# Kernel optimization log

Measured on AMD Instinct MI355X. Metric: run time of the kernel, lower is better.

## Reference

```python
import jax, jax.numpy as jnp
import numpy as np

DIM = 1024
HEADS = 16
HEAD_DIM = DIM // HEADS
RANK = 16
ALPHA = 8.0
SCALING = ALPHA / RANK  # 0.5
SCALE = HEAD_DIM ** (-0.5)
B_, L_ = 2, 2048


def _proj_params(key, std=0.02):
    kW, kb, kA, kB = jax.random.split(key, 4)
    W = jax.random.normal(kW, (DIM, DIM), jnp.float32) * std   # [out, in]
    b = jax.random.normal(kb, (DIM,), jnp.float32) * std
    A = jax.random.normal(kA, (DIM, RANK), jnp.float32) * std  # [out, r]
    Bm = jax.random.normal(kB, (RANK, DIM), jnp.float32) * std # [r, in]
    return W, b, A, Bm


def setup_inputs() -> dict:
    key = jax.random.key(0)
    ks = jax.random.split(key, 6)
    x = jax.random.normal(ks[0], (B_, L_, DIM), jnp.float32)
    attn_bias = jax.random.normal(ks[1], (1, HEADS, L_, L_), jnp.float32) * 0.1
    inp = {"x": x, "attn_bias": attn_bias}
    for name, k in zip("qkvo", ks[2:6]):
        W, b, A, Bm = _proj_params(k)
        inp[f"W{name}"] = W
        inp[f"b{name}"] = b
        inp[f"A{name}"] = A
        inp[f"B{name}"] = Bm
    return inp


def _lora_linear(x, W, b, A, Bm):
    # y = x W^T + b + scaling * ((x @ A) @ B)   (matches torch LoRALinear)
    return x @ W.T + b + SCALING * ((x @ A) @ Bm)


def _split(x):
    B, L, D = x.shape
    return jnp.swapaxes(x.reshape(B, L, HEADS, HEAD_DIM), 1, 2)  # [B,H,L,hd]


def reference(x, attn_bias, Wq, bq, Aq, Bq, Wk, bk, Ak, Bk, Wv, bv, Av, Bv, Wo, bo, Ao, Bo):
    B, L, D = x.shape
    q = _split(_lora_linear(x, Wq, bq, Aq, Bq))
    k = _split(_lora_linear(x, Wk, bk, Ak, Bk))
    v = _split(_lora_linear(x, Wv, bv, Av, Bv))
    scores = jnp.einsum('bhld,bhmd->bhlm', q, k) * SCALE + attn_bias
    attn = jax.nn.softmax(scores, axis=-1)  # dropout p=0 -> identity
    out = jnp.einsum('bhlm,bhmd->bhld', attn, v)
    out = jnp.swapaxes(out, 1, 2).reshape(B, L, D)  # merge heads
    return _lora_linear(out, Wo, bo, Ao, Bo)
```

## Files before the change

kernel.cpp:

```cpp
#include <hip/hip_runtime.h>
#include <cstdint>

typedef __bf16 bf16;
typedef __bf16 bf16x8 __attribute__((ext_vector_type(8)));
typedef __bf16 bf16x4 __attribute__((ext_vector_type(4)));
typedef float  f32x4  __attribute__((ext_vector_type(4)));
typedef float  f32x16 __attribute__((ext_vector_type(16)));
typedef int    i32x4  __attribute__((ext_vector_type(4)));

#define DIM   1024
#define LSEQ  2048
#define NH    16
#define HD    64
#define NTOK  4096

#define AS1C(p) ((const __attribute__((address_space(1))) void*)(unsigned long long)(uintptr_t)(p))
#define AS3P(p) ((__attribute__((address_space(3))) void*)(unsigned int)(uintptr_t)(p))
#define SB0 __builtin_amdgcn_sched_barrier(0)
#define CPOL_NT 2

__device__ __forceinline__ f32x4 mfma16(bf16x8 a, bf16x8 b, f32x4 c) {
  return __builtin_amdgcn_mfma_f32_16x16x32_bf16(a, b, c, 0, 0, 0);
}
__device__ __forceinline__ f32x16 mfma32(bf16x8 a, bf16x8 b, f32x16 c) {
  return __builtin_amdgcn_mfma_f32_32x32x16_bf16(a, b, c, 0, 0, 0);
}
__device__ __forceinline__ int pk2(float a, float b) {
  unsigned short ua = __builtin_bit_cast(unsigned short, (bf16)a);
  unsigned short ub = __builtin_bit_cast(unsigned short, (bf16)b);
  return (int)ua | ((int)ub << 16);
}

__global__ __launch_bounds__(256) void k_cvt(const float* __restrict__ x,
                                             bf16* __restrict__ xb) {
  const int i = (blockIdx.x * 256 + threadIdx.x) * 4;
  const f32x4 v = *(const f32x4*)(x + i);
  bf16x4 o;
  o[0] = (bf16)v[0]; o[1] = (bf16)v[1]; o[2] = (bf16)v[2]; o[3] = (bf16)v[3];
  *(bf16x4*)(xb + i) = o;
}

struct WeffArgs {
  const float* W[4]; const float* A[4]; const float* B[4]; bf16* out[4];
};

__global__ __launch_bounds__(256) void k_weff(WeffArgs args) {
  const int o = blockIdx.x;
  const int z = blockIdx.y;
  const float* __restrict__ W  = args.W[z];
  const float* __restrict__ A  = args.A[z];
  const float* __restrict__ Bm = args.B[z];
  bf16* __restrict__ out = args.out[z];
  float Bo[16];
#pragma unroll
  for (int r = 0; r < 16; ++r) Bo[r] = Bm[r * DIM + o];
#pragma unroll
  for (int j = 0; j < 4; ++j) {
    const int d = j * 256 + (int)threadIdx.x;
    const float* Ar = A + (size_t)d * 16;
    float acc = 0.f;
#pragma unroll
    for (int r = 0; r < 16; ++r) acc += Ar[r] * Bo[r];
    out[(size_t)o * DIM + d] = (bf16)(W[(size_t)o * DIM + d] + 0.5f * acc);
  }
}

template <int NF, bool F32OUT>
__device__ __forceinline__ void gemm_body64(const bf16* __restrict__ X,
                                            const bf16* __restrict__ W,
                                            const float* __restrict__ bias,
                                            void* __restrict__ out,
                                            float scale, int m0, int n0, int ncol0) {
  constexpr int BN = NF * 32;
  constexpr int BJ = BN / 32;
  __shared__ __align__(16) bf16 As[128 * 64];
  __shared__ __align__(16) bf16 Bs[BN * 64];
  const int tid  = threadIdx.x;
  const int lane = tid & 63, w = tid >> 6;
  const int l15 = lane & 15, l4 = lane >> 4;
  const int wr = w >> 1, wc = w & 1;
  const int lr = lane >> 3;
  const int scol = ((lane & 7) ^ lr) * 8;

  f32x4 acc[4][NF] = {};
  const bf16* ag = X + (size_t)m0 * DIM;
  const bf16* bg = W + (size_t)n0 * DIM;

  for (int kt = 0; kt < DIM / 64; ++kt) {
    const int k0 = kt * 64;
#pragma unroll
    for (int j = 0; j < 4; ++j) {
      const int rb = w * 4 + j;
      __builtin_amdgcn_global_load_lds(
          AS1C(ag + (size_t)(rb * 8 + lr) * DIM + k0 + scol),
          AS3P(As + rb * 512), 16, 0, 0);
    }
#pragma unroll
    for (int j = 0; j < BJ; ++j) {
      const int rb = w * BJ + j;
      __builtin_amdgcn_global_load_lds(
          AS1C(bg + (size_t)(rb * 8 + lr) * DIM + k0 + scol),
          AS3P(Bs + rb * 512), 16, 0, 0);
    }
    __syncthreads();
    bf16x8 af[2][4], bfr[2][NF];
#pragma unroll
    for (int ks = 0; ks < 2; ++ks) {
#pragma unroll
      for (int m = 0; m < 4; ++m) {
        const int r = wr * 64 + m * 16 + l15;
        af[ks][m] = *(const bf16x8*)(As + r * 64 + ((ks * 4 + l4) ^ (r & 7)) * 8);
      }
#pragma unroll
      for (int n = 0; n < NF; ++n) {
        const int r = wc * (NF * 16) + n * 16 + l15;
        bfr[ks][n] = *(const bf16x8*)(Bs + r * 64 + ((ks * 4 + l4) ^ (r & 7)) * 8);
      }
    }
#pragma unroll
    for (int m = 0; m < 4; ++m)
#pragma unroll
      for (int n = 0; n < NF; ++n) {
        acc[m][n] = mfma16(af[0][m], bfr[0][n], acc[m][n]);
        acc[m][n] = mfma16(af[1][m], bfr[1][n], acc[m][n]);
      }
    __syncthreads();
  }

#pragma unroll
  for (int m = 0; m < 4; ++m) {
    const int r0 = m0 + wr * 64 + m * 16 + l4 * 4;
#pragma unroll
    for (int n = 0; n < NF; ++n) {
      const int c = ncol0 + wc * (NF * 16) + n * 16 + l15;
      const float bc = bias[c];
#pragma unroll
      for (int t = 0; t < 4; ++t) {
        const float y = (acc[m][n][t] + bc) * scale;
        if constexpr (F32OUT)
          ((float*)out)[(size_t)(r0 + t) * DIM + c] = y;
        else
          ((bf16*)out)[(size_t)(r0 + t) * DIM + c] = (bf16)y;
      }
    }
  }
}

__global__ __launch_bounds__(256) void k_gemm_qkv(
    const bf16* __restrict__ xb, const bf16* __restrict__ weff,
    const float* __restrict__ bq, const float* __restrict__ bk,
    const float* __restrict__ bv,
    bf16* __restrict__ q, bf16* __restrict__ k, bf16* __restrict__ v) {
  const int n0 = blockIdx.y * 128;
  const int z = n0 >> 10;
  const float* bias = (z == 0) ? bq : (z == 1) ? bk : bv;
  bf16* out = (z == 0) ? q : (z == 1) ? k : v;
  const float scale = (z == 0) ? 0.125f : 1.0f;
  gemm_body64<4, false>(xb, weff, bias, out, scale, blockIdx.x * 128, n0, n0 & 1023);
}

__global__ __launch_bounds__(256) void k_gemm_o(
    const bf16* __restrict__ ctx, const bf16* __restrict__ weffo,
    const float* __restrict__ bo, float* __restrict__ out) {
  const int n0 = blockIdx.y * 64;
  gemm_body64<2, true>(ctx, weffo, bo, out, 1.0f, blockIdx.x * 128, n0, n0);
}

__global__ __launch_bounds__(256) void k_vfrag(const bf16* __restrict__ v,
                                               const bf16* __restrict__ k,
                                               bf16* __restrict__ vf,
                                               bf16* __restrict__ kf) {
  const int lt = blockIdx.x, bh = blockIdx.y;
  const int b = bh >> 4, h = bh & 15;
  __shared__ __align__(16) bf16 tile[64][72];
  const int tid = threadIdx.x;
  const int r = tid >> 2, c0 = (tid & 3) * 16;
  const bf16* src = v + (size_t)(b * LSEQ + lt * 64) * DIM + h * HD;
  *(bf16x8*)(&tile[r][c0])     = *(const bf16x8*)(src + (size_t)r * DIM + c0);
  *(bf16x8*)(&tile[r][c0 + 8]) = *(const bf16x8*)(src + (size_t)r * DIM + c0 + 8);
  __syncthreads();
  const int w = tid >> 6, lane = tid & 63, l31 = lane & 31, hi = lane >> 5;
  {
    const int tt = w >> 1, n = w & 1;
    const int t = lt * 2 + tt;
#pragma unroll
    for (int c = 0; c < 2; ++c) {
      bf16 tmp[8];
#pragma unroll
      for (int j = 0; j < 8; ++j)
        tmp[j] = tile[tt * 32 + c * 16 + hi * 8 + j][n * 32 + l31];
      *(bf16x8*)(vf + ((((size_t)bh * 64 + t) * 4 + n * 2 + c) * 64 + lane) * 8) =
          *(bf16x8*)tmp;
    }
  }
  {
    const int t = lt * 2 + (w & 1);
    const bf16* krow = k + (size_t)(b * LSEQ + t * 32 + l31) * DIM + h * HD + hi * 8;
#pragma unroll
    for (int cc = 0; cc < 2; ++cc) {
      const int c = (w >> 1) + cc * 2;
      *(bf16x8*)(kf + ((((size_t)bh * 64 + t) * 4 + c) * 64 + lane) * 8) =
          *(const bf16x8*)(krow + c * 16);
    }
  }
}

__global__ __launch_bounds__(512, 4) void k_attn(
    const bf16* __restrict__ q, const bf16* __restrict__ kf,
    const bf16* __restrict__ vf, const float* __restrict__ bias,
    bf16* __restrict__ ctx) {
  const int tid = threadIdx.x, w = tid >> 6, lane = tid & 63;
  const int l31 = lane & 31, hi = lane >> 5;
  const int bb = w >> 2, qs = w & 3;
  const int h = blockIdx.x & 15;
  const int q0 = (blockIdx.x >> 4) * 128;

  __shared__ __align__(16) bf16  kls[2][2][2048];
  __shared__ __align__(16) bf16  vls[2][2][2048];
  __shared__ __align__(16) float bls[3][4096];

  const bf16* qrow = q + (size_t)(bb * LSEQ + q0 + qs * 32 + l31) * DIM + h * HD;
  bf16x8 Qf[4];
#pragma unroll
  for (int c = 0; c < 4; ++c) Qf[c] = *(const bf16x8*)(qrow + c * 16 + hi * 8);

  const int kvA = 2 * w, kvB = 2 * w + 1;
  const int kbA = kvA >> 3, vvA = (kvA >> 2) & 1, cA = kvA & 3;
  const int kbB = kvB >> 3, vvB = (kvB >> 2) & 1, cB = kvB & 3;
  const bf16* srcA = (vvA ? vf : kf) + (size_t)(kbA * NH + h) * 64 * 2048 + cA * 512 + lane * 8;
  const bf16* srcB = (vvB ? vf : kf) + (size_t)(kbB * NH + h) * 64 * 2048 + cB * 512 + lane * 8;
  bf16* dstA = (vvA ? &vls[kbA][0][0] : &kls[kbA][0][0]) + cA * 512 + lane * 8;
  bf16* dstB = (vvB ? &vls[kbB][0][0] : &kls[kbB][0][0]) + cB * 512 + lane * 8;
  const int lr = lane >> 3, lc = lane & 7;
  const float* bsA = bias + ((size_t)h * LSEQ + q0 + 16 * w + lr) * LSEQ + 4 * (lc ^ lr);
  const float* bsB = bsA + (size_t)8 * LSEQ;
  float* bdA = &bls[0][0] + (2 * w) * 256 + lane * 4;
  float* bdB = bdA + 256;

  f32x16 acc0 = {}, acc1 = {};
  float mrun = -3e38f, lrun = 0.f;

#define STAGEKV(t_, s_)                                                        \
  {                                                                            \
    __builtin_amdgcn_global_load_lds(AS1C(srcA + (size_t)(t_) * 2048),         \
                                     AS3P(dstA + (s_) * 2048), 16, 0, 0);      \
    __builtin_amdgcn_global_load_lds(AS1C(srcB + (size_t)(t_) * 2048),         \
                                     AS3P(dstB + (s_) * 2048), 16, 0, 0);      \
  }
#define STAGEB(t_, s_)                                                         \
  {                                                                            \
    __builtin_amdgcn_global_load_lds(AS1C(bsA + (size_t)(t_) * 32),            \
                                     AS3P(bdA + (s_) * 4096), 16, 0, CPOL_NT); \
    __builtin_amdgcn_global_load_lds(AS1C(bsB + (size_t)(t_) * 32),            \
                                     AS3P(bdB + (s_) * 4096), 16, 0, CPOL_NT); \
  }

  STAGEKV(0, 0); SB0;
  STAGEB(0, 0); SB0;
  STAGEB(1, 1); SB0;

  const int rr = qs * 32 + l31;
  const int sw = (l31 & 7) << 2;
  for (int t = 0; t < 64; ++t) {
    const int slKV = t & 1;
    const int slB = t % 3;
    { const int tn = (t + 1 > 63) ? 63 : t + 1; STAGEKV(tn, (t + 1) & 1); } SB0;
    { const int tn = (t + 2 > 63) ? 63 : t + 2; STAGEB(tn, (t + 2) % 3); } SB0;
    asm volatile("s_waitcnt vmcnt(6)" ::: "memory");
    __builtin_amdgcn_s_barrier();

    bf16x8 Kf[4], Vf[2][2];
    f32x4 br[4];
#pragma unroll
    for (int c = 0; c < 4; ++c)
      Kf[c] = *(const bf16x8*)(&kls[bb][slKV][c * 512 + lane * 8]);
#pragma unroll
    for (int u = 0; u < 4; ++u)
      Vf[u >> 1][u & 1] = *(const bf16x8*)(&vls[bb][slKV][u * 512 + lane * 8]);
#pragma unroll
    for (int g = 0; g < 4; ++g)
      br[g] = *(const f32x4*)(
          &bls[slB][rr * 32 + (((g << 3) | (hi << 2)) ^ sw)]);
    asm volatile("s_waitcnt lgkmcnt(0)" ::: "memory");
    SB0;
    __builtin_amdgcn_s_barrier();

    f32x16 s = {};
#pragma unroll
    for (int c = 0; c < 4; ++c) s = mfma32(Kf[c], Qf[c], s);
    float p[16];
#pragma unroll
    for (int r = 0; r < 16; ++r) p[r] = s[r] + br[r >> 2][r & 3];
    float m8[8];
#pragma unroll
    for (int i = 0; i < 8; ++i) m8[i] = fmaxf(p[i], p[i + 8]);
    float tm = fmaxf(fmaxf(fmaxf(m8[0], m8[4]), fmaxf(m8[1], m8[5])),
                     fmaxf(fmaxf(m8[2], m8[6]), fmaxf(m8[3], m8[7])));
    tm = fmaxf(tm, __shfl_xor(tm, 32));
    if (!__all(tm <= mrun + 8.0f)) {
      const float mn = fmaxf(mrun, tm);
      const float scl = __expf(mrun - mn);
      mrun = mn;
      lrun *= scl;
#pragma unroll
      for (int r = 0; r < 16; ++r) { acc0[r] *= scl; acc1[r] *= scl; }
    }
#pragma unroll
    for (int r = 0; r < 16; ++r) p[r] = __expf(p[r] - mrun);
    float s8[8];
#pragma unroll
    for (int i = 0; i < 8; ++i) s8[i] = p[i] + p[i + 8];
    float rs = ((s8[0] + s8[1]) + (s8[2] + s8[3])) + ((s8[4] + s8[5]) + (s8[6] + s8[7]));
    rs += __shfl_xor(rs, 32);
    lrun += rs;
#pragma unroll
    for (int c = 0; c < 2; ++c) {
      const int c8 = c * 8;
      const int A0 = pk2(p[c8 + 0], p[c8 + 1]);
      const int A1 = pk2(p[c8 + 2], p[c8 + 3]);
      const int B0 = pk2(p[c8 + 4], p[c8 + 5]);
      const int B1 = pk2(p[c8 + 6], p[c8 + 7]);
      const int pA0 = __shfl_xor(A0, 32), pA1 = __shfl_xor(A1, 32);
      const int pB0 = __shfl_xor(B0, 32), pB1 = __shfl_xor(B1, 32);
      i32x4 fi;
      fi[0] = hi ? pB0 : A0;
      fi[1] = hi ? pB1 : A1;
      fi[2] = hi ? B0 : pA0;
      fi[3] = hi ? B1 : pA1;
      const bf16x8 pf = __builtin_bit_cast(bf16x8, fi);
      acc0 = mfma32(Vf[0][c], pf, acc0);
      acc1 = mfma32(Vf[1][c], pf, acc1);
    }
  }
#undef STAGEKV
#undef STAGEB

  const float inv = 1.0f / lrun;
  bf16* cp = ctx + (size_t)(bb * LSEQ + q0 + qs * 32 + l31) * DIM + h * HD;
#pragma unroll
  for (int r = 0; r < 16; ++r) {
    const int dr = (r & 3) + 8 * (r >> 2) + 4 * hi;
    cp[dr]      = (bf16)(acc0[r] * inv);
    cp[32 + dr] = (bf16)(acc1[r] * inv);
  }
}

extern "C" void kernel_launch(void* const* d_in, const int* in_sizes, int n_in,
                              void* d_out, int out_size, void* d_ws, size_t ws_size,
                              hipStream_t stream) {
  const float* x  = (const float*)d_in[0];
  const float* ab = (const float*)d_in[1];
  const float* Wq = (const float*)d_in[2];  const float* bq = (const float*)d_in[3];
  const float* Aq = (const float*)d_in[4];  const float* Bq = (const float*)d_in[5];
  const float* Wk = (const float*)d_in[6];  const float* bk = (const float*)d_in[7];
  const float* Ak = (const float*)d_in[8];  const float* Bk = (const float*)d_in[9];
  const float* Wv = (const float*)d_in[10]; const float* bv = (const float*)d_in[11];
  const float* Av = (const float*)d_in[12]; const float* Bv = (const float*)d_in[13];
  const float* Wo = (const float*)d_in[14]; const float* bo = (const float*)d_in[15];
  const float* Ao = (const float*)d_in[16]; const float* Bo = (const float*)d_in[17];

  uint8_t* ws = (uint8_t*)d_ws;
  const size_t SZ = (size_t)NTOK * DIM * sizeof(bf16);
  bf16* xb   = (bf16*)(ws + 0 * SZ);
  bf16* weff = (bf16*)(ws + 1 * SZ);
  bf16* qb   = (bf16*)(ws + 2 * SZ);
  bf16* kb   = (bf16*)(ws + 3 * SZ);
  bf16* vb   = (bf16*)(ws + 4 * SZ);
  bf16* kfb  = (bf16*)(ws + 5 * SZ);
  bf16* vfb  = (bf16*)(ws + 6 * SZ);
  bf16* ctx  = (bf16*)(ws + 7 * SZ);

  k_cvt<<<dim3(NTOK * DIM / 1024), 256, 0, stream>>>(x, xb);

  WeffArgs wa;
  wa.W[0] = Wq; wa.A[0] = Aq; wa.B[0] = Bq; wa.out[0] = weff;
  wa.W[1] = Wk; wa.A[1] = Ak; wa.B[1] = Bk; wa.out[1] = weff + (size_t)DIM * DIM;
  wa.W[2] = Wv; wa.A[2] = Av; wa.B[2] = Bv; wa.out[2] = weff + 2 * (size_t)DIM * DIM;
  wa.W[3] = Wo; wa.A[3] = Ao; wa.B[3] = Bo; wa.out[3] = weff + 3 * (size_t)DIM * DIM;
  k_weff<<<dim3(DIM, 4), 256, 0, stream>>>(wa);

  k_gemm_qkv<<<dim3(32, 24), 256, 0, stream>>>(xb, weff, bq, bk, bv, qb, kb, vb);
  k_vfrag<<<dim3(32, 32), 256, 0, stream>>>(vb, kb, vfb, kfb);
  k_attn<<<dim3(256), 512, 0, stream>>>(qb, kfb, vfb, ab, ctx);
  k_gemm_o<<<dim3(32, 16), 256, 0, stream>>>(ctx, weff + 3 * (size_t)DIM * DIM, bo,
                                             (float*)d_out);
}
```

Baseline: 190.0 us.

## Process two query groups per wave in attention to reuse K/V tiles

Each attention block now covers 256 query rows, with every wave computing two 32-row query groups against the same staged K/V fragments. The grid drops to 128 blocks, the bias staging buffer doubles, and the load wait count is raised to match. The aim is to halve K/V global-to-LDS traffic and barrier overhead per query. In exchange it uses more registers and LDS, lowers occupancy (launch bounds set to 1), and launches fewer blocks than there are CUs.

```diff
diff --git a/kernel.cpp b/kernel.cpp
--- a/kernel.cpp
+++ b/kernel.cpp
@@ -205,7 +205,7 @@
   }
 }
 
-__global__ __launch_bounds__(512, 4) void k_attn(
+__global__ __launch_bounds__(512, 1) void k_attn(
     const bf16* __restrict__ q, const bf16* __restrict__ kf,
     const bf16* __restrict__ vf, const float* __restrict__ bias,
     bf16* __restrict__ ctx) {
@@ -213,16 +213,20 @@
   const int l31 = lane & 31, hi = lane >> 5;
   const int bb = w >> 2, qs = w & 3;
   const int h = blockIdx.x & 15;
-  const int q0 = (blockIdx.x >> 4) * 128;
+  const int q0 = (blockIdx.x >> 4) * 256;
 
   __shared__ __align__(16) bf16  kls[2][2][2048];
   __shared__ __align__(16) bf16  vls[2][2][2048];
-  __shared__ __align__(16) float bls[3][4096];
-
-  const bf16* qrow = q + (size_t)(bb * LSEQ + q0 + qs * 32 + l31) * DIM + h * HD;
-  bf16x8 Qf[4];
-#pragma unroll
-  for (int c = 0; c < 4; ++c) Qf[c] = *(const bf16x8*)(qrow + c * 16 + hi * 8);
+  __shared__ __align__(16) float bls[3][8192];
+
+  bf16x8 Qf[2][4];
+#pragma unroll
+  for (int g = 0; g < 2; ++g) {
+    const bf16* qrow =
+        q + (size_t)(bb * LSEQ + q0 + qs * 64 + g * 32 + l31) * DIM + h * HD;
+#pragma unroll
+    for (int c = 0; c < 4; ++c) Qf[g][c] = *(const bf16x8*)(qrow + c * 16 + hi * 8);
+  }
 
   const int kvA = 2 * w, kvB = 2 * w + 1;
   const int kbA = kvA >> 3, vvA = (kvA >> 2) & 1, cA = kvA & 3;
@@ -231,14 +235,19 @@
   const bf16* srcB = (vvB ? vf : kf) + (size_t)(kbB * NH + h) * 64 * 2048 + cB * 512 + lane * 8;
   bf16* dstA = (vvA ? &vls[kbA][0][0] : &kls[kbA][0][0]) + cA * 512 + lane * 8;
   bf16* dstB = (vvB ? &vls[kbB][0][0] : &kls[kbB][0][0]) + cB * 512 + lane * 8;
+
   const int lr = lane >> 3, lc = lane & 7;
-  const float* bsA = bias + ((size_t)h * LSEQ + q0 + 16 * w + lr) * LSEQ + 4 * (lc ^ lr);
-  const float* bsB = bsA + (size_t)8 * LSEQ;
-  float* bdA = &bls[0][0] + (2 * w) * 256 + lane * 4;
-  float* bdB = bdA + 256;
-
-  f32x16 acc0 = {}, acc1 = {};
-  float mrun = -3e38f, lrun = 0.f;
+  const float* bs0 = bias + ((size_t)h * LSEQ + q0 + 32 * w + lr) * LSEQ + 4 * (lc ^ lr);
+  const float* bs1 = bs0 + (size_t)8 * LSEQ;
+  const float* bs2 = bs0 + (size_t)16 * LSEQ;
+  const float* bs3 = bs0 + (size_t)24 * LSEQ;
+  float* bd0 = &bls[0][0] + (4 * w) * 256 + lane * 4;
+  float* bd1 = bd0 + 256;
+  float* bd2 = bd0 + 512;
+  float* bd3 = bd0 + 768;
+
+  f32x16 acc0[2] = {}, acc1[2] = {};
+  float mrun[2] = {-3e38f, -3e38f}, lrun[2] = {0.f, 0.f};
 
 #define STAGEKV(t_, s_)                                                        \
   {                                                                            \
@@ -249,28 +258,31 @@
   }
 #define STAGEB(t_, s_)                                                         \
   {                                                                            \
-    __builtin_amdgcn_global_load_lds(AS1C(bsA + (size_t)(t_) * 32),            \
-                                     AS3P(bdA + (s_) * 4096), 16, 0, CPOL_NT); \
-    __builtin_amdgcn_global_load_lds(AS1C(bsB + (size_t)(t_) * 32),            \
-                                     AS3P(bdB + (s_) * 4096), 16, 0, CPOL_NT); \
+    __builtin_amdgcn_global_load_lds(AS1C(bs0 + (size_t)(t_) * 32),            \
+                                     AS3P(bd0 + (s_) * 8192), 16, 0, CPOL_NT); \
+    __builtin_amdgcn_global_load_lds(AS1C(bs1 + (size_t)(t_) * 32),            \
+                                     AS3P(bd1 + (s_) * 8192), 16, 0, CPOL_NT); \
+    __builtin_amdgcn_global_load_lds(AS1C(bs2 + (size_t)(t_) * 32),            \
+                                     AS3P(bd2 + (s_) * 8192), 16, 0, CPOL_NT); \
+    __builtin_amdgcn_global_load_lds(AS1C(bs3 + (size_t)(t_) * 32),            \
+                                     AS3P(bd3 + (s_) * 8192), 16, 0, CPOL_NT); \
   }
 
   STAGEKV(0, 0); SB0;
   STAGEB(0, 0); SB0;
   STAGEB(1, 1); SB0;
 
-  const int rr = qs * 32 + l31;
   const int sw = (l31 & 7) << 2;
   for (int t = 0; t < 64; ++t) {
     const int slKV = t & 1;
     const int slB = t % 3;
     { const int tn = (t + 1 > 63) ? 63 : t + 1; STAGEKV(tn, (t + 1) & 1); } SB0;
     { const int tn = (t + 2 > 63) ? 63 : t + 2; STAGEB(tn, (t + 2) % 3); } SB0;
-    asm volatile("s_waitcnt vmcnt(6)" ::: "memory");
+    asm volatile("s_waitcnt vmcnt(10)" ::: "memory");
     __builtin_amdgcn_s_barrier();
 
     bf16x8 Kf[4], Vf[2][2];
-    f32x4 br[4];
+    f32x4 br[2][4];
 #pragma unroll
     for (int c = 0; c < 4; ++c)
       Kf[c] = *(const bf16x8*)(&kls[bb][slKV][c * 512 + lane * 8]);
@@ -278,70 +290,80 @@
     for (int u = 0; u < 4; ++u)
       Vf[u >> 1][u & 1] = *(const bf16x8*)(&vls[bb][slKV][u * 512 + lane * 8]);
 #pragma unroll
-    for (int g = 0; g < 4; ++g)
-      br[g] = *(const f32x4*)(
-          &bls[slB][rr * 32 + (((g << 3) | (hi << 2)) ^ sw)]);
+    for (int g = 0; g < 2; ++g) {
+      const int rr = qs * 64 + g * 32 + l31;
+#pragma unroll
+      for (int gg = 0; gg < 4; ++gg)
+        br[g][gg] = *(const f32x4*)(
+            &bls[slB][rr * 32 + (((gg << 3) | (hi << 2)) ^ sw)]);
+    }
     asm volatile("s_waitcnt lgkmcnt(0)" ::: "memory");
     SB0;
     __builtin_amdgcn_s_barrier();
 
-    f32x16 s = {};
-#pragma unroll
-    for (int c = 0; c < 4; ++c) s = mfma32(Kf[c], Qf[c], s);
-    float p[16];
-#pragma unroll
-    for (int r = 0; r < 16; ++r) p[r] = s[r] + br[r >> 2][r & 3];
-    float m8[8];
-#pragma unroll
-    for (int i = 0; i < 8; ++i) m8[i] = fmaxf(p[i], p[i + 8]);
-    float tm = fmaxf(fmaxf(fmaxf(m8[0], m8[4]), fmaxf(m8[1], m8[5])),
-                     fmaxf(fmaxf(m8[2], m8[6]), fmaxf(m8[3], m8[7])));
-    tm = fmaxf(tm, __shfl_xor(tm, 32));
-    if (!__all(tm <= mrun + 8.0f)) {
-      const float mn = fmaxf(mrun, tm);
-      const float scl = __expf(mrun - mn);
-      mrun = mn;
-      lrun *= scl;
-#pragma unroll
-      for (int r = 0; r < 16; ++r) { acc0[r] *= scl; acc1[r] *= scl; }
-    }
-#pragma unroll
-    for (int r = 0; r < 16; ++r) p[r] = __expf(p[r] - mrun);
-    float s8[8];
-#pragma unroll
-    for (int i = 0; i < 8; ++i) s8[i] = p[i] + p[i + 8];
-    float rs = ((s8[0] + s8[1]) + (s8[2] + s8[3])) + ((s8[4] + s8[5]) + (s8[6] + s8[7]));
-    rs += __shfl_xor(rs, 32);
-    lrun += rs;
-#pragma unroll
-    for (int c = 0; c < 2; ++c) {
-      const int c8 = c * 8;
-      const int A0 = pk2(p[c8 + 0], p[c8 + 1]);
-      const int A1 = pk2(p[c8 + 2], p[c8 + 3]);
-      const int B0 = pk2(p[c8 + 4], p[c8 + 5]);
-      const int B1 = pk2(p[c8 + 6], p[c8 + 7]);
-      const int pA0 = __shfl_xor(A0, 32), pA1 = __shfl_xor(A1, 32);
-      const int pB0 = __shfl_xor(B0, 32), pB1 = __shfl_xor(B1, 32);
-      i32x4 fi;
-      fi[0] = hi ? pB0 : A0;
-      fi[1] = hi ? pB1 : A1;
-      fi[2] = hi ? B0 : pA0;
-      fi[3] = hi ? B1 : pA1;
-      const bf16x8 pf = __builtin_bit_cast(bf16x8, fi);
-      acc0 = mfma32(Vf[0][c], pf, acc0);
-      acc1 = mfma32(Vf[1][c], pf, acc1);
+#pragma unroll
+    for (int g = 0; g < 2; ++g) {
+      f32x16 s = {};
+#pragma unroll
+      for (int c = 0; c < 4; ++c) s = mfma32(Kf[c], Qf[g][c], s);
+      float p[16];
+#pragma unroll
+      for (int r = 0; r < 16; ++r) p[r] = s[r] + br[g][r >> 2][r & 3];
+      float m8[8];
+#pragma unroll
+      for (int i = 0; i < 8; ++i) m8[i] = fmaxf(p[i], p[i + 8]);
+      float tm = fmaxf(fmaxf(fmaxf(m8[0], m8[4]), fmaxf(m8[1], m8[5])),
+                       fmaxf(fmaxf(m8[2], m8[6]), fmaxf(m8[3], m8[7])));
+      tm = fmaxf(tm, __shfl_xor(tm, 32));
+      if (!__all(tm <= mrun[g] + 8.0f)) {
+        const float mn = fmaxf(mrun[g], tm);
+        const float scl = __expf(mrun[g] - mn);
+        mrun[g] = mn;
+        lrun[g] *= scl;
+#pragma unroll
+        for (int r = 0; r < 16; ++r) { acc0[g][r] *= scl; acc1[g][r] *= scl; }
+      }
+#pragma unroll
+      for (int r = 0; r < 16; ++r) p[r] = __expf(p[r] - mrun[g]);
+      float s8[8];
+#pragma unroll
+      for (int i = 0; i < 8; ++i) s8[i] = p[i] + p[i + 8];
+      float rs = ((s8[0] + s8[1]) + (s8[2] + s8[3])) + ((s8[4] + s8[5]) + (s8[6] + s8[7]));
+      rs += __shfl_xor(rs, 32);
+      lrun[g] += rs;
+#pragma unroll
+      for (int c = 0; c < 2; ++c) {
+        const int c8 = c * 8;
+        const int A0 = pk2(p[c8 + 0], p[c8 + 1]);
+        const int A1 = pk2(p[c8 + 2], p[c8 + 3]);
+        const int B0 = pk2(p[c8 + 4], p[c8 + 5]);
+        const int B1 = pk2(p[c8 + 6], p[c8 + 7]);
+        const int pA0 = __shfl_xor(A0, 32), pA1 = __shfl_xor(A1, 32);
+        const int pB0 = __shfl_xor(B0, 32), pB1 = __shfl_xor(B1, 32);
+        i32x4 fi;
+        fi[0] = hi ? pB0 : A0;
+        fi[1] = hi ? pB1 : A1;
+        fi[2] = hi ? B0 : pA0;
+        fi[3] = hi ? B1 : pA1;
+        const bf16x8 pf = __builtin_bit_cast(bf16x8, fi);
+        acc0[g] = mfma32(Vf[0][c], pf, acc0[g]);
+        acc1[g] = mfma32(Vf[1][c], pf, acc1[g]);
+      }
     }
   }
 #undef STAGEKV
 #undef STAGEB
 
-  const float inv = 1.0f / lrun;
-  bf16* cp = ctx + (size_t)(bb * LSEQ + q0 + qs * 32 + l31) * DIM + h * HD;
-#pragma unroll
-  for (int r = 0; r < 16; ++r) {
-    const int dr = (r & 3) + 8 * (r >> 2) + 4 * hi;
-    cp[dr]      = (bf16)(acc0[r] * inv);
-    cp[32 + dr] = (bf16)(acc1[r] * inv);
+#pragma unroll
+  for (int g = 0; g < 2; ++g) {
+    const float inv = 1.0f / lrun[g];
+    bf16* cp = ctx + (size_t)(bb * LSEQ + q0 + qs * 64 + g * 32 + l31) * DIM + h * HD;
+#pragma unroll
+    for (int r = 0; r < 16; ++r) {
+      const int dr = (r & 3) + 8 * (r >> 2) + 4 * hi;
+      cp[dr]      = (bf16)(acc0[g][r] * inv);
+      cp[32 + dr] = (bf16)(acc1[g][r] * inv);
+    }
   }
 }
 
@@ -381,7 +403,7 @@
 
   k_gemm_qkv<<<dim3(32, 24), 256, 0, stream>>>(xb, weff, bq, bk, bv, qb, kb, vb);
   k_vfrag<<<dim3(32, 32), 256, 0, stream>>>(vb, kb, vfb, kfb);
-  k_attn<<<dim3(256), 512, 0, stream>>>(qb, kfb, vfb, ab, ctx);
+  k_attn<<<dim3(128), 512, 0, stream>>>(qb, kfb, vfb, ab, ctx);
   k_gemm_o<<<dim3(32, 16), 256, 0, stream>>>(ctx, weff + 3 * (size_t)DIM * DIM, bo,
                                              (float*)d_out);
 }
```

After: 211.5 us. 11.3% more time.
